# Optimization experiments

Measured on AMD Instinct MI355X. Metric: run time of the kernel, lower is better.

Reference implementation:

```python
import jax, jax.numpy as jnp
import numpy as np
from jax import lax

N_J = 53
N_NAMES = 18
C_IN, C_OUT, K = 32, 32, 3
B, T = 16, 2048
# joint -> unique-name id (first-occurrence order of RELATED_NODES values)
NAME_IDS = np.array([0,1,2,3,4,1,2,3,4,5,6,7,8,9,10,11,12,13,14,15,16,14,15,16,14,15,16,14,15,16,14,15,16,10,11,12,13,14,15,16,14,15,16,14,15,16,14,15,16,14,15,16,17])
# adjacency: each joint attends to [self, parent] (uniform degree 2)
ADJ = np.array([[i, max(i - 1, 0)] for i in range(N_J)])


def setup_inputs() -> dict:
    key = jax.random.key(0)
    ks = jax.random.split(key, 5)
    return {
        "x": jax.random.normal(ks[0], (B, T, N_J, C_IN), jnp.float32),
        "lin_w": jax.random.normal(ks[1], (N_NAMES, 2 * C_IN, C_OUT), jnp.float32) / np.sqrt(2 * C_IN).astype(np.float32),
        "lin_b": jax.random.normal(ks[2], (N_NAMES, C_OUT), jnp.float32) * 0.01,
        "conv_w": jax.random.normal(ks[3], (N_NAMES, C_OUT, C_OUT, K), jnp.float32) / np.sqrt(C_OUT * K).astype(np.float32),
        "conv_b": jax.random.normal(ks[4], (N_NAMES, C_OUT), jnp.float32) * 0.01,
    }


def reference(x, lin_w, lin_b, conv_w, conv_b):
    Bb, Tt = x.shape[0], x.shape[1]
    # per-joint gather of [self, parent] neighbors: [B,T,J,2,Cin]
    gath = x[:, :, ADJ, :]
    feat = gath.reshape(Bb, Tt, N_J, 2 * C_IN)
    # shared-by-name Linear weights, gathered per joint
    Wj = lin_w[NAME_IDS]  # [J, 2Cin, Cout]
    bj = lin_b[NAME_IDS]  # [J, Cout]
    h = jax.nn.relu(jnp.einsum('btjf,jfo->btjo', feat, Wj) + bj)  # [B,T,J,Cout]
    # reflect-pad time axis (torch Conv1d padding_mode='reflect', padding=1)
    hp = jnp.pad(h, ((0, 0), (1, 1), (0, 0), (0, 0)), mode='reflect')
    # grouped 1D conv: one group per joint with its name's kernel
    hc = hp.transpose(0, 2, 3, 1).reshape(Bb, N_J * C_OUT, Tt + 2)  # [B, J*Cout, T+2]
    kw = conv_w[NAME_IDS].reshape(N_J * C_OUT, C_OUT, K)            # [J*Cout, Cout, K]
    y = lax.conv_general_dilated(hc, kw, (1,), 'VALID',
                                 dimension_numbers=('NCH', 'OIH', 'NCH'),
                                 feature_group_count=N_J)           # [B, J*Cout, T]
    y = y.reshape(Bb, N_J, C_OUT, Tt) + conv_b[NAME_IDS][None, :, :, None]
    return y.transpose(0, 3, 1, 2)  # [B, T, J, Cout]
```

## Files before the change

### kernel.cpp

```cpp
#include <hip/hip_runtime.h>
#include <hip/hip_bf16.h>
#include <cstddef>
#include <cstdint>

typedef __attribute__((ext_vector_type(8))) short short8_t;
typedef __attribute__((ext_vector_type(4))) float f32x4;
typedef unsigned short ushort4a __attribute__((ext_vector_type(4)));

#define WAVE_FENCE()                                        \
  do {                                                      \
    asm volatile("s_waitcnt lgkmcnt(0)" ::: "memory");      \
    __builtin_amdgcn_sched_barrier(0);                      \
  } while (0)
#define VM_FENCE()                                          \
  do {                                                      \
    asm volatile("s_waitcnt vmcnt(0)" ::: "memory");        \
    __builtin_amdgcn_sched_barrier(0);                      \
  } while (0)

namespace {
constexpr int T = 2048;
constexpr int NB = 16;
constexpr int NJ = 53;
constexpr int NN = 18;
constexpr int TTILE = 128;
constexpr int NTILES = T / TTILE;
constexpr int MT_LIN = 9;
constexpr int MT_CNV = 8;
constexpr int HROWS = MT_LIN * 16;
constexpr int HSTR = 36;
constexpr int SSTR = 40;
constexpr int NBLK = NB * NJ * NTILES;
constexpr int XSPAN = NBLK / 8;
}

__constant__ int c_name_ids[NJ] = {
    0,1,2,3,4,1,2,3,4,5,6,7,8,9,10,11,12,13,14,15,16,14,15,16,14,15,16,
    14,15,16,14,15,16,10,11,12,13,14,15,16,14,15,16,14,15,16,14,15,16,
    14,15,16,17};

__device__ short8_t g_linfrag[NN][2][2][2][64];
__device__ short8_t g_convfrag[NN][3][2][2][64];

__device__ __forceinline__ unsigned short f2bf(float f) {
  return __builtin_bit_cast(unsigned short, __float2bfloat16(f));
}
__device__ __forceinline__ float bf2f(unsigned short u) {
  return __bfloat162float(__builtin_bit_cast(__hip_bfloat16, u));
}


__global__ __launch_bounds__(64)
void prep_weights(const float* __restrict__ lin_w,
                  const float* __restrict__ conv_w)
{
  const int n = blockIdx.x;
  const int l = threadIdx.x;
  const int r = l & 15;
  const int g = l >> 4;
#pragma unroll
  for (int ks = 0; ks < 2; ++ks)
#pragma unroll
    for (int nt = 0; nt < 2; ++nt) {
      short8_t hi8, lo8;
#pragma unroll
      for (int e = 0; e < 8; ++e) {
        const int kk = 4 * g + (e & 3) + 16 * (e >> 2);
        const float w = lin_w[((size_t)n * 64 + ks * 32 + kk) * 32 + r + 16 * nt];
        const unsigned short h = f2bf(w);
        hi8[e] = (short)h;
        lo8[e] = (short)f2bf(w - bf2f(h));
      }
      g_linfrag[n][ks][nt][0][l] = hi8;
      g_linfrag[n][ks][nt][1][l] = lo8;
    }
#pragma unroll
  for (int k = 0; k < 3; ++k)
#pragma unroll
    for (int nt = 0; nt < 2; ++nt) {
      short8_t hi8, lo8;
#pragma unroll
      for (int e = 0; e < 8; ++e) {
        const int i = 4 * g + (e & 3) + 16 * (e >> 2);
        const float w = conv_w[(((size_t)n * 32 + r + 16 * nt) * 32 + i) * 3 + k];
        const unsigned short h = f2bf(w);
        hi8[e] = (short)h;
        lo8[e] = (short)f2bf(w - bf2f(h));
      }
      g_convfrag[n][k][nt][0][l] = hi8;
      g_convfrag[n][k][nt][1][l] = lo8;
    }
}

__global__ __launch_bounds__(256, 4)
void fused_rcb_mfma(const float* __restrict__ x,
                    const float* __restrict__ lin_b,
                    const float* __restrict__ conv_b,
                    float* __restrict__ out)
{
  __shared__ __align__(16) unsigned short s_hi[HROWS * HSTR];
  __shared__ __align__(16) char s_feat[4][4096];

  const int raw = blockIdx.x;
  const int bid = (raw % 8) * XSPAN + (raw / 8);
  const int j    = bid % NJ;
  const int tile = (bid / NJ) % NTILES;
  const int b    = bid / (NJ * NTILES);
  const int nid  = c_name_ids[j];
  const int jp   = (j > 0) ? (j - 1) : 0;
  const int t0   = tile * TTILE;

  const int tid = threadIdx.x;
  const int wv = tid >> 6;
  const int l  = tid & 63;
  const int r  = l & 15;
  const int g  = l >> 4;

  char* featc = s_feat[wv];

  const float* xj_base = x + ((size_t)b * T * NJ + j) * 32;
  const float* xp_base = x + ((size_t)b * T * NJ + jp) * 32;

  short8_t blh[2][2], bll[2][2];
#pragma unroll
  for (int ks = 0; ks < 2; ++ks)
#pragma unroll
    for (int nt = 0; nt < 2; ++nt) {
      blh[ks][nt] = g_linfrag[nid][ks][nt][0][l];
      bll[ks][nt] = g_linfrag[nid][ks][nt][1][l];
    }
  const float lb0 = lin_b[nid * 32 + r];
  const float lb1 = lin_b[nid * 32 + r + 16];

  auto issue_feat = [&](int mt) {
#pragma unroll
    for (int j2 = 0; j2 < 2; ++j2) {
      const float* jb = j2 ? xp_base : xj_base;
#pragma unroll
      for (int i = 0; i < 2; ++i) {
        const int row = i * 8 + (l >> 3);
        int t = t0 + mt * 16 + row - 1;
        if (t < 0) t = -t;
        if (t > T - 1) t = 2 * (T - 1) - t;
        const char* src = reinterpret_cast<const char*>(jb + (size_t)t * (NJ * 32))
                          + (((l & 7) * 16) ^ ((row & 7) << 4));
        __builtin_amdgcn_global_load_lds(
            (const __attribute__((address_space(1))) unsigned int*)src,
            (__attribute__((address_space(3))) unsigned int*)(&s_feat[wv][j2 * 2048 + i * 1024]),
            16, 0, 0);
      }
    }
  };

  issue_feat(wv);
  for (int mt = wv; mt < MT_LIN; mt += 4) {
    VM_FENCE();

    short8_t ah[2], al[2];
#pragma unroll
    for (int ks = 0; ks < 2; ++ks) {
      const char* fw = featc + ks * 2048 + r * 128;
      const f32x4 a0 = *reinterpret_cast<const f32x4*>(fw + ((16 * g) ^ ((r & 7) << 4)));
      const f32x4 a1 = *reinterpret_cast<const f32x4*>(fw + ((64 + 16 * g) ^ ((r & 7) << 4)));
#pragma unroll
      for (int e = 0; e < 8; ++e) {
        const float f = (e < 4) ? a0[e] : a1[e - 4];
        const unsigned short h = f2bf(f);
        ah[ks][e] = (short)h;
        al[ks][e] = (short)f2bf(f - bf2f(h));
      }
    }
    WAVE_FENCE();
    if (mt + 4 < MT_LIN) issue_feat(mt + 4);

#pragma unroll
    for (int nt = 0; nt < 2; ++nt) {
      const float lb = nt ? lb1 : lb0;
      f32x4 acc = {lb, lb, lb, lb};
#pragma unroll
      for (int ks = 0; ks < 2; ++ks) {
        acc = __builtin_amdgcn_mfma_f32_16x16x32_bf16(ah[ks], blh[ks][nt], acc, 0, 0, 0);
        acc = __builtin_amdgcn_mfma_f32_16x16x32_bf16(al[ks], blh[ks][nt], acc, 0, 0, 0);
        acc = __builtin_amdgcn_mfma_f32_16x16x32_bf16(ah[ks], bll[ks][nt], acc, 0, 0, 0);
      }
#pragma unroll
      for (int q = 0; q < 4; ++q) {
        const int hrow = mt * 16 + 4 * g + q;
        s_hi[hrow * HSTR + r + 16 * nt] = f2bf(fmaxf(acc[q], 0.0f));
      }
    }
  }
  __syncthreads();

  short8_t bch[3][2], bcl[3][2];
#pragma unroll
  for (int k = 0; k < 3; ++k)
#pragma unroll
    for (int nt = 0; nt < 2; ++nt) {
      bch[k][nt] = g_convfrag[nid][k][nt][0][l];
      bcl[k][nt] = g_convfrag[nid][k][nt][1][l];
    }
  const float cb0 = conv_b[nid * 32 + r];
  const float cb1 = conv_b[nid * 32 + r + 16];

  float* st = reinterpret_cast<float*>(featc);

  for (int mt = wv; mt < MT_CNV; mt += 4) {
    const int m0 = mt * 16;
    short8_t ah[3];
#pragma unroll
    for (int k = 0; k < 3; ++k) {
      const int arow = m0 + r + k;
      const ushort4a u0 = *reinterpret_cast<const ushort4a*>(&s_hi[arow * HSTR + 4 * g]);
      const ushort4a u1 = *reinterpret_cast<const ushort4a*>(&s_hi[arow * HSTR + 16 + 4 * g]);
      short8_t hi8;
#pragma unroll
      for (int e = 0; e < 4; ++e) {
        hi8[e] = (short)u0[e];
        hi8[e + 4] = (short)u1[e];
      }
      ah[k] = hi8;
    }

    f32x4 accv[2];
#pragma unroll
    for (int nt = 0; nt < 2; ++nt) {
      const float cb = nt ? cb1 : cb0;
      f32x4 acc = {cb, cb, cb, cb};
#pragma unroll
      for (int k = 0; k < 3; ++k) {
        acc = __builtin_amdgcn_mfma_f32_16x16x32_bf16(ah[k], bch[k][nt], acc, 0, 0, 0);
        acc = __builtin_amdgcn_mfma_f32_16x16x32_bf16(ah[k], bcl[k][nt], acc, 0, 0, 0);
      }
      accv[nt] = acc;
    }

    WAVE_FENCE();
#pragma unroll
    for (int nt = 0; nt < 2; ++nt)
#pragma unroll
      for (int q = 0; q < 4; ++q)
        st[(4 * g + q) * SSTR + r + 16 * nt] = accv[nt][q];
    WAVE_FENCE();

#pragma unroll
    for (int h2 = 0; h2 < 2; ++h2) {
      const int row = h2 * 8 + (l >> 3);
      const f32x4 rd = *reinterpret_cast<const f32x4*>(
          st + row * SSTR + (l & 7) * 4);
      const int t = t0 + m0 + row;
      __builtin_nontemporal_store(rd, reinterpret_cast<f32x4*>(
          out + ((size_t)(b * T + t) * NJ + j) * 32 + (l & 7) * 4));
    }
  }
}

extern "C" void kernel_launch(void* const* d_in, const int* in_sizes, int n_in,
                              void* d_out, int out_size, void* d_ws, size_t ws_size,
                              hipStream_t stream) {
  const float* x      = (const float*)d_in[0];
  const float* lin_w  = (const float*)d_in[1];
  const float* lin_b  = (const float*)d_in[2];
  const float* conv_w = (const float*)d_in[3];
  const float* conv_b = (const float*)d_in[4];
  float* out = (float*)d_out;

  prep_weights<<<dim3(NN), 64, 0, stream>>>(lin_w, conv_w);
  fused_rcb_mfma<<<dim3(NBLK), 256, 0, stream>>>(x, lin_b, conv_b, out);
}
```

Measured before the change: 87.52 us.

## Load x directly into registers, shrink LDS footprint, and raise occupancy

```diff
diff --git a/kernel.cpp b/kernel.cpp
--- a/kernel.cpp
+++ b/kernel.cpp
@@ -5,16 +5,12 @@
 
 typedef __attribute__((ext_vector_type(8))) short short8_t;
 typedef __attribute__((ext_vector_type(4))) float f32x4;
+typedef __attribute__((ext_vector_type(2))) float f32x2;
 typedef unsigned short ushort4a __attribute__((ext_vector_type(4)));
 
 #define WAVE_FENCE()                                        \
   do {                                                      \
     asm volatile("s_waitcnt lgkmcnt(0)" ::: "memory");      \
-    __builtin_amdgcn_sched_barrier(0);                      \
-  } while (0)
-#define VM_FENCE()                                          \
-  do {                                                      \
-    asm volatile("s_waitcnt vmcnt(0)" ::: "memory");        \
     __builtin_amdgcn_sched_barrier(0);                      \
   } while (0)
 
@@ -27,9 +23,9 @@
 constexpr int NTILES = T / TTILE;
 constexpr int MT_LIN = 9;
 constexpr int MT_CNV = 8;
-constexpr int HROWS = MT_LIN * 16;
+constexpr int HROWS = TTILE + 2;
 constexpr int HSTR = 36;
-constexpr int SSTR = 40;
+constexpr int SSTR = 38;
 constexpr int NBLK = NB * NJ * NTILES;
 constexpr int XSPAN = NBLK / 8;
 }
@@ -92,14 +88,14 @@
     }
 }
 
-__global__ __launch_bounds__(256, 4)
+__global__ __launch_bounds__(256, 7)
 void fused_rcb_mfma(const float* __restrict__ x,
                     const float* __restrict__ lin_b,
                     const float* __restrict__ conv_b,
                     float* __restrict__ out)
 {
   __shared__ __align__(16) unsigned short s_hi[HROWS * HSTR];
-  __shared__ __align__(16) char s_feat[4][4096];
+  __shared__ __align__(16) float s_st[4][16 * SSTR];
 
   const int raw = blockIdx.x;
   const int bid = (raw % 8) * XSPAN + (raw / 8);
@@ -116,8 +112,6 @@
   const int r  = l & 15;
   const int g  = l >> 4;
 
-  char* featc = s_feat[wv];
-
   const float* xj_base = x + ((size_t)b * T * NJ + j) * 32;
   const float* xp_base = x + ((size_t)b * T * NJ + jp) * 32;
 
@@ -132,46 +126,31 @@
   const float lb0 = lin_b[nid * 32 + r];
   const float lb1 = lin_b[nid * 32 + r + 16];
 
-  auto issue_feat = [&](int mt) {
-#pragma unroll
-    for (int j2 = 0; j2 < 2; ++j2) {
-      const float* jb = j2 ? xp_base : xj_base;
-#pragma unroll
-      for (int i = 0; i < 2; ++i) {
-        const int row = i * 8 + (l >> 3);
-        int t = t0 + mt * 16 + row - 1;
-        if (t < 0) t = -t;
-        if (t > T - 1) t = 2 * (T - 1) - t;
-        const char* src = reinterpret_cast<const char*>(jb + (size_t)t * (NJ * 32))
-                          + (((l & 7) * 16) ^ ((row & 7) << 4));
-        __builtin_amdgcn_global_load_lds(
-            (const __attribute__((address_space(1))) unsigned int*)src,
-            (__attribute__((address_space(3))) unsigned int*)(&s_feat[wv][j2 * 2048 + i * 1024]),
-            16, 0, 0);
-      }
-    }
-  };
-
-  issue_feat(wv);
   for (int mt = wv; mt < MT_LIN; mt += 4) {
-    VM_FENCE();
+    int t = t0 + mt * 16 + r - 1;
+    t = (t < 0) ? -t : t;
+    t = (t > T - 1) ? (2 * (T - 1) - t) : t;
+    const float* rowj = xj_base + (size_t)t * (NJ * 32);
+    const float* rowp = xp_base + (size_t)t * (NJ * 32);
+    f32x4 v00 = *reinterpret_cast<const f32x4*>(rowj + 4 * g);
+    f32x4 v01 = *reinterpret_cast<const f32x4*>(rowj + 16 + 4 * g);
+    f32x4 v10 = *reinterpret_cast<const f32x4*>(rowp + 4 * g);
+    f32x4 v11 = *reinterpret_cast<const f32x4*>(rowp + 16 + 4 * g);
 
     short8_t ah[2], al[2];
 #pragma unroll
     for (int ks = 0; ks < 2; ++ks) {
-      const char* fw = featc + ks * 2048 + r * 128;
-      const f32x4 a0 = *reinterpret_cast<const f32x4*>(fw + ((16 * g) ^ ((r & 7) << 4)));
-      const f32x4 a1 = *reinterpret_cast<const f32x4*>(fw + ((64 + 16 * g) ^ ((r & 7) << 4)));
+      const f32x4 a0 = ks ? v10 : v00;
+      const f32x4 a1 = ks ? v11 : v01;
 #pragma unroll
       for (int e = 0; e < 8; ++e) {
         const float f = (e < 4) ? a0[e] : a1[e - 4];
-        const unsigned short h = f2bf(f);
-        ah[ks][e] = (short)h;
-        al[ks][e] = (short)f2bf(f - bf2f(h));
-      }
-    }
-    WAVE_FENCE();
-    if (mt + 4 < MT_LIN) issue_feat(mt + 4);
+        const uint32_t bi = __builtin_bit_cast(uint32_t, f);
+        ah[ks][e] = (short)(unsigned short)(bi >> 16);
+        const float lo = f - __builtin_bit_cast(float, bi & 0xffff0000u);
+        al[ks][e] = (short)f2bf(lo);
+      }
+    }
 
 #pragma unroll
     for (int nt = 0; nt < 2; ++nt) {
@@ -186,7 +165,8 @@
 #pragma unroll
       for (int q = 0; q < 4; ++q) {
         const int hrow = mt * 16 + 4 * g + q;
-        s_hi[hrow * HSTR + r + 16 * nt] = f2bf(fmaxf(acc[q], 0.0f));
+        if (hrow < HROWS)
+          s_hi[hrow * HSTR + r + 16 * nt] = f2bf(fmaxf(acc[q], 0.0f));
       }
     }
   }
@@ -203,7 +183,7 @@
   const float cb0 = conv_b[nid * 32 + r];
   const float cb1 = conv_b[nid * 32 + r + 16];
 
-  float* st = reinterpret_cast<float*>(featc);
+  float* st = s_st[wv];
 
   for (int mt = wv; mt < MT_CNV; mt += 4) {
     const int m0 = mt * 16;
@@ -246,8 +226,11 @@
 #pragma unroll
     for (int h2 = 0; h2 < 2; ++h2) {
       const int row = h2 * 8 + (l >> 3);
-      const f32x4 rd = *reinterpret_cast<const f32x4*>(
-          st + row * SSTR + (l & 7) * 4);
+      const float* rp = st + row * SSTR + (l & 7) * 4;
+      const f32x2 rd0 = *reinterpret_cast<const f32x2*>(rp);
+      const f32x2 rd1 = *reinterpret_cast<const f32x2*>(rp + 2);
+      f32x4 rd;
+      rd[0] = rd0[0]; rd[1] = rd0[1]; rd[2] = rd1[0]; rd[3] = rd1[1];
       const int t = t0 + m0 + row;
       __builtin_nontemporal_store(rd, reinterpret_cast<f32x4*>(
           out + ((size_t)(b * T + t) * NJ + j) * 32 + (l & 7) * 4));
```

Result: slower. 177.0 us (+102.2%).
